# Kernel tuning notes

Measured on AMD Instinct MI355X. Metric: run time of the kernel, lower is better.

## Reference

```python
import jax, jax.numpy as jnp
import numpy as np

B, L, F, E, D, N_OUT, FC = 2048, 100, 64, 256, 256, 3, 128


def _lstm_cell(x, h, c, Wi, Wh, b):
    gates = x @ Wi + h @ Wh + b  # (B, 4H)
    i, f, g, o = jnp.split(gates, 4, axis=-1)
    c_new = jax.nn.sigmoid(f) * c + jax.nn.sigmoid(i) * jnp.tanh(g)
    h_new = jax.nn.sigmoid(o) * jnp.tanh(c_new)
    return h_new, c_new


def setup_inputs() -> dict:
    key = jax.random.key(0)
    ks = jax.random.split(key, 12)
    s = 0.05
    return {
        "x": jax.random.normal(ks[0], (B, L, F), jnp.float32),
        # encoder input-attention (shared across timesteps, as in [layer]*look_back)
        "Wa": jax.random.normal(ks[1], (F + E, F), jnp.float32) * s,
        "ba": jnp.zeros((F,), jnp.float32),
        # encoder LSTM cell
        "Wi": jax.random.normal(ks[2], (F, 4 * E), jnp.float32) * s,
        "Wh": jax.random.normal(ks[3], (E, 4 * E), jnp.float32) * s,
        "be": jnp.zeros((4 * E,), jnp.float32),
        # decoder temporal attention
        "Wd": jax.random.normal(ks[4], (E + D, D), jnp.float32) * s,
        "bd": jnp.zeros((D,), jnp.float32),
        "Wl": jax.random.normal(ks[5], (D, 1), jnp.float32) * s,
        "bl": jnp.zeros((1,), jnp.float32),
        # decoder LSTM cell
        "Wdi": jax.random.normal(ks[6], (E, 4 * D), jnp.float32) * s,
        "Wdh": jax.random.normal(ks[7], (D, 4 * D), jnp.float32) * s,
        "bdec": jnp.zeros((4 * D,), jnp.float32),
        # output head: tanh(D->FC) then tanh(FC->1)
        "Wf": jax.random.normal(ks[8], (D, FC), jnp.float32) * s,
        "bf": jnp.zeros((FC,), jnp.float32),
        "Wo": jax.random.normal(ks[9], (FC, 1), jnp.float32) * s,
        "bo": jnp.zeros((1,), jnp.float32),
    }


def reference(x, Wa, ba, Wi, Wh, be, Wd, bd, Wl, bl, Wdi, Wdh, bdec, Wf, bf, Wo, bo):
    # ---------- encoder: per-timestep input attention + LSTM cell ----------
    x_t = jnp.transpose(x, (1, 0, 2))  # (L, B, F)

    def enc_step(carry, xt):
        h, c = carry
        energies = jnp.tanh(jnp.concatenate([xt, h], axis=1) @ Wa + ba)  # (B, F)
        a = jax.nn.softmax(energies, axis=1)
        enc_in = a * xt  # attended input (B, F)
        h, c = _lstm_cell(enc_in, h, c, Wi, Wh, be)
        return (h, c), h

    h0 = jnp.zeros((B, E), x.dtype)
    c0 = jnp.zeros((B, E), x.dtype)
    _, enc_out = jax.lax.scan(enc_step, (h0, c0), x_t)  # (L, B, E)

    # ---------- decoder: temporal attention over encoder states + LSTM ----------
    h_d = jnp.zeros((B, D), x.dtype)
    c_d = jnp.zeros((B, D), x.dtype)
    outs = []
    for _ in range(N_OUT):  # small fixed output horizon
        con = jnp.broadcast_to(h_d[None, :, :], (L, B, D))
        en = jnp.tanh(jnp.concatenate([enc_out, con], axis=2) @ Wd + bd)  # (L, B, D)
        scores = en @ Wl + bl  # (L, B, 1)
        alpha = jax.nn.softmax(scores, axis=0)  # over time
        ctx = jnp.sum(alpha * enc_out, axis=0)  # (B, E)
        h_d, c_d = _lstm_cell(ctx, h_d, c_d, Wdi, Wdh, bdec)
        fc = jnp.tanh(h_d @ Wf + bf)  # (B, FC)
        outs.append(jnp.tanh(fc @ Wo + bo))  # (B, 1)
    return jnp.concatenate(outs, axis=1)  # (B, n_output)
```

## Files before the change

kernel.cpp:

```cpp
#include <hip/hip_runtime.h>
#include <math.h>

#define BB 2048
#define LL 100
#define FF 64
#define EE 256
#define DD 256
#define NOUT 3

#define COMP(v, i) ((i) == 0 ? (v).x : (i) == 1 ? (v).y : (i) == 2 ? (v).z : (v).w)

typedef unsigned short u16;
typedef unsigned int u32;
typedef __attribute__((ext_vector_type(8))) __bf16 bf16x8;
typedef __attribute__((ext_vector_type(4))) float f32x4;
typedef __attribute__((ext_vector_type(2))) float f32x2;

#define MFMA_(A, B, C) __builtin_amdgcn_mfma_f32_16x16x32_bf16((A), (B), (C), 0, 0, 0)

__device__ __forceinline__ float sigmoidf_(float x) {
    return 1.0f / (1.0f + expf(-x));
}
__device__ __forceinline__ float tanhf_(float x) {
    return 1.0f - 2.0f / (1.0f + expf(2.0f * x));
}
__device__ __forceinline__ u16 f2b_(float f) {
    u32 u = __float_as_uint(f);
    u = (u + 0x7FFFu + ((u >> 16) & 1u)) >> 16;
    return (u16)u;
}
__device__ __forceinline__ float b2f_(u16 b) {
    return __uint_as_float(((u32)b) << 16);
}
__device__ __forceinline__ u32 pack2_(float a, float b) {
    return (u32)f2b_(a) | ((u32)f2b_(b) << 16);
}
__device__ __forceinline__ f32x4 splat4(float b) {
    f32x4 v; v[0] = b; v[1] = b; v[2] = b; v[3] = b; return v;
}
__device__ __forceinline__ void split8(const float* v, uint4& H, uint4& L) {
    u16 h[8], lo[8];
    #pragma unroll
    for (int e = 0; e < 8; ++e) {
        h[e]  = f2b_(v[e]);
        lo[e] = f2b_(v[e] - b2f_(h[e]));
    }
    H = make_uint4((u32)h[0]  | ((u32)h[1]  << 16), (u32)h[2]  | ((u32)h[3]  << 16),
                   (u32)h[4]  | ((u32)h[5]  << 16), (u32)h[6]  | ((u32)h[7]  << 16));
    L = make_uint4((u32)lo[0] | ((u32)lo[1] << 16), (u32)lo[2] | ((u32)lo[3] << 16),
                   (u32)lo[4] | ((u32)lo[5] << 16), (u32)lo[6] | ((u32)lo[7] << 16));
}

#define AF(mt, kt, p, ln) (((((mt) * 10 + (kt)) * 2 + (p)) * 64 + (ln)) * 8)
#define AFX(mt, kt, p, ln) AF(mt, kt, p, (ln) ^ (((ln) >> 4) & 3))
#define AF2(mt, kt, p, ln) (((((mt) * 8 + (kt)) * 2 + (p)) * 64 + (ln)) * 8)

__global__ __launch_bounds__(64) void w_prep_all(
    const float* __restrict__ Wi, const float* __restrict__ Wh,
    const float* __restrict__ Wa, const float* __restrict__ Wd,
    u16* __restrict__ wp)
{
    const int bid = blockIdx.x;
    const int l   = threadIdx.x;

    float v[8];
    if (bid < 640) {
        const int nt = bid / 10, kt = bid - nt * 10;
        const int col = nt * 16 + (l & 15);
        #pragma unroll
        for (int e = 0; e < 8; ++e) {
            const int k = kt * 32 + ((l >> 4) << 3) + e;
            v[e] = (k < 64) ? Wi[(size_t)k * 1024 + col]
                            : Wh[(size_t)(k - 64) * 1024 + col];
        }
    } else if (bid < 680) {
        const int b2 = bid - 640;
        const int nt = b2 / 10, kt = b2 - nt * 10;
        const int col = nt * 16 + (l & 15);
        #pragma unroll
        for (int e = 0; e < 8; ++e) {
            const int k = kt * 32 + ((l >> 4) << 3) + e;
            v[e] = Wa[(size_t)k * 64 + col];
        }
    } else {
        const int b2 = bid - 680;
        const int nt = b2 >> 3, kt = b2 & 7;
        const int col = nt * 16 + (l & 15);
        #pragma unroll
        for (int e = 0; e < 8; ++e) {
            const int k = kt * 32 + ((l >> 4) << 3) + e;
            v[e] = Wd[(size_t)k * 256 + col];
        }
    }
    uint4 H, L;
    split8(v, H, L);
    *(uint4*)&wp[(size_t)bid * 1024 + (size_t)l * 8]       = H;
    *(uint4*)&wp[(size_t)bid * 1024 + 512 + (size_t)l * 8] = L;
}

__global__ __launch_bounds__(1024) void enc_mfma4(
    const float* __restrict__ x,
    const float* __restrict__ ba, const float* __restrict__ be,
    const u16* __restrict__ wp,
    float* __restrict__ enc_out,
    float* __restrict__ hbuf,
    u32* __restrict__ flags)
{
    __shared__ u16   aFrag[20480];
    __shared__ float x_s[32 * 68];
    __shared__ float e_s[32 * 68];
    __shared__ float gate_s[4][32][66];

    const int bid = blockIdx.x;
    const int g   = (bid & 7) | ((bid >> 5) << 3);
    const int p   = (bid >> 3) & 3;
    const int row0 = g * 32;
    const int tid = threadIdx.x;
    const int l   = tid & 63;
    const int w   = tid >> 6;

    for (int v = tid; v < 20480 / 2; v += 1024) ((u32*)aFrag)[v] = 0u;

    const int ntW = (w >> 2) * 16 + p * 4 + (w & 3);
    uint4 BhR[10];
    #pragma unroll
    for (int kt = 0; kt < 10; ++kt)
        BhR[kt] = *(const uint4*)&wp[(size_t)(ntW * 10 + kt) * 1024 + (size_t)l * 8];

    const float be_r = be[(size_t)ntW * 16 + (l & 15)];
    const float ba_r = (w < 8) ? ba[(w & 3) * 16 + (l & 15)] : 0.f;

    float c_state[2] = {0.f, 0.f};

    __syncthreads();

    for (int t = 0; t < LL; ++t) {
        if (t > 0) {
            if (tid == 0) {
                const u32 target = 4u * (u32)t;
                int guard = 0;
                while (__hip_atomic_load(&flags[g * 32], __ATOMIC_RELAXED,
                                         __HIP_MEMORY_SCOPE_AGENT) < target) {
                    __builtin_amdgcn_s_sleep(1);
                    if (++guard > 2000000) break;
                }
            }
            __syncthreads();
        }

        if (tid < 256) {
            const int kt2 = tid >> 7;
            const int mt  = (tid >> 6) & 1;
            const int l2  = tid & 63;
            const int row2 = mt * 16 + (l2 & 15);
            const int f0   = kt2 * 32 + ((l2 >> 4) << 3);
            const float* xp = x + (size_t)(row0 + row2) * (LL * FF) + (size_t)t * FF + f0;
            float4 xa = *(const float4*)xp;
            float4 xb = *(const float4*)(xp + 4);
            float v[8] = {xa.x, xa.y, xa.z, xa.w, xb.x, xb.y, xb.z, xb.w};
            uint4 H, L;
            split8(v, H, L);
            *(uint4*)&aFrag[AFX(mt, kt2, 0, l2)] = H;
            *(uint4*)&aFrag[AFX(mt, kt2, 1, l2)] = L;
            *(float4*)&x_s[row2 * 68 + f0]     = xa;
            *(float4*)&x_s[row2 * 68 + f0 + 4] = xb;
        } else if (t > 0) {
            const int v   = tid - 256;
            const int prl = v >> 8;
            const int vv  = v & 255;
            const int row = vv >> 3;
            const int i8  = vv & 7;
            const int ugp = (p + 1 + prl) & 3;
            const int u8  = ugp * 64 + i8 * 8;
            const float* hp_g = hbuf + ((size_t)((t - 1) & 1) * BB + row0 + row) * 256 + u8;
            f32x4 a4, b4;
            asm volatile("global_load_dwordx4 %0, %2, off sc0 sc1\n\t"
                         "global_load_dwordx4 %1, %3, off sc0 sc1\n\t"
                         "s_waitcnt vmcnt(0)"
                         : "=v"(a4), "=v"(b4)
                         : "v"(hp_g), "v"(hp_g + 4) : "memory");
            float v8[8] = {a4[0], a4[1], a4[2], a4[3], b4[0], b4[1], b4[2], b4[3]};
            uint4 H, L;
            split8(v8, H, L);
            const int mt = row >> 4, rowT = row & 15;
            const int kt_h = 2 + (u8 >> 5);
            const int g2   = (u8 & 31) >> 3;
            const int ln   = rowT + (g2 << 4);
            *(uint4*)&aFrag[AFX(mt, kt_h, 0, ln)] = H;
            *(uint4*)&aFrag[AFX(mt, kt_h, 1, ln)] = L;
        }
        __syncthreads();

        f32x4 acc0, acc1;

        if (w < 8) {
            const int mt  = w >> 2;
            const int nta = w & 3;
            f32x4 ea = splat4(ba_r);
            #pragma unroll
            for (int kt = 0; kt < 10; ++kt) {
                bf16x8 Ah = *(const bf16x8*)&aFrag[AFX(mt, kt, 0, l)];
                bf16x8 Al = *(const bf16x8*)&aFrag[AFX(mt, kt, 1, l)];
                const size_t o = (size_t)(640 + nta * 10 + kt) * 1024 + (size_t)l * 8;
                bf16x8 Bh = *(const bf16x8*)&wp[o];
                bf16x8 Bl = *(const bf16x8*)&wp[o + 512];
                ea = MFMA_(Ah, Bh, ea);
                ea = MFMA_(Al, Bh, ea);
                ea = MFMA_(Ah, Bl, ea);
            }
            const int colA = nta * 16 + (l & 15);
            #pragma unroll
            for (int r = 0; r < 4; ++r) {
                const int rowT = ((l >> 4) << 2) + r;
                e_s[(mt * 16 + rowT) * 68 + colA] = tanhf_(ea[r]);
            }
        } else {
            acc0 = splat4(be_r); acc1 = splat4(be_r);
            #pragma unroll
            for (int kt = 2; kt < 10; ++kt) {
                bf16x8 Ah0 = *(const bf16x8*)&aFrag[AFX(0, kt, 0, l)];
                bf16x8 Al0 = *(const bf16x8*)&aFrag[AFX(0, kt, 1, l)];
                bf16x8 Ah1 = *(const bf16x8*)&aFrag[AFX(1, kt, 0, l)];
                bf16x8 Al1 = *(const bf16x8*)&aFrag[AFX(1, kt, 1, l)];
                bf16x8 Bl  = *(const bf16x8*)&wp[(size_t)(ntW * 10 + kt) * 1024 + 512 + (size_t)l * 8];
                bf16x8 Bh  = __builtin_bit_cast(bf16x8, BhR[kt]);
                acc0 = MFMA_(Ah0, Bh, acc0);
                acc1 = MFMA_(Ah1, Bh, acc1);
                acc0 = MFMA_(Al0, Bh, acc0);
                acc1 = MFMA_(Al1, Bh, acc1);
                acc0 = MFMA_(Ah0, Bl, acc0);
                acc1 = MFMA_(Ah1, Bl, acc1);
            }
        }
        __syncthreads();

        if (w >= 8) {
            const int v2   = tid - 512;
            const int row2 = v2 >> 4;
            const int c4   = (v2 & 15) * 4;
            float4 ev = *(const float4*)&e_s[row2 * 68 + c4];
            float m = fmaxf(fmaxf(ev.x, ev.y), fmaxf(ev.z, ev.w));
            #pragma unroll
            for (int msk = 8; msk >= 1; msk >>= 1) m = fmaxf(m, __shfl_xor(m, msk, 64));
            float4 ex;
            ex.x = expf(ev.x - m); ex.y = expf(ev.y - m);
            ex.z = expf(ev.z - m); ex.w = expf(ev.w - m);
            float s = ex.x + ex.y + ex.z + ex.w;
            #pragma unroll
            for (int msk = 8; msk >= 1; msk >>= 1) s += __shfl_xor(s, msk, 64);
            const float inv = 1.f / s;
            float4 xv = *(const float4*)&x_s[row2 * 68 + c4];
            float ein[4] = { ex.x * inv * xv.x, ex.y * inv * xv.y,
                             ex.z * inv * xv.z, ex.w * inv * xv.w };
            const int mt   = row2 >> 4;
            const int rowT = row2 & 15;
            const int kt   = c4 >> 5;
            const int g2   = (c4 & 31) >> 3;
            const int e0   = c4 & 7;
            const int ln   = rowT + (g2 << 4);
            ushort4 h4, l4;
            #pragma unroll
            for (int e = 0; e < 4; ++e) {
                u16 hh = f2b_(ein[e]);
                u16 ll = f2b_(ein[e] - b2f_(hh));
                if (e == 0) { h4.x = hh; l4.x = ll; } else if (e == 1) { h4.y = hh; l4.y = ll; }
                else if (e == 2) { h4.z = hh; l4.z = ll; } else { h4.w = hh; l4.w = ll; }
            }
            *(ushort4*)&aFrag[AFX(mt, kt, 0, ln) + e0] = h4;
            *(ushort4*)&aFrag[AFX(mt, kt, 1, ln) + e0] = l4;
        } else {
            acc0 = splat4(be_r); acc1 = splat4(be_r);
            #pragma unroll
            for (int kt = 2; kt < 10; ++kt) {
                bf16x8 Ah0 = *(const bf16x8*)&aFrag[AFX(0, kt, 0, l)];
                bf16x8 Al0 = *(const bf16x8*)&aFrag[AFX(0, kt, 1, l)];
                bf16x8 Ah1 = *(const bf16x8*)&aFrag[AFX(1, kt, 0, l)];
                bf16x8 Al1 = *(const bf16x8*)&aFrag[AFX(1, kt, 1, l)];
                bf16x8 Bl  = *(const bf16x8*)&wp[(size_t)(ntW * 10 + kt) * 1024 + 512 + (size_t)l * 8];
                bf16x8 Bh  = __builtin_bit_cast(bf16x8, BhR[kt]);
                acc0 = MFMA_(Ah0, Bh, acc0);
                acc1 = MFMA_(Ah1, Bh, acc1);
                acc0 = MFMA_(Al0, Bh, acc0);
                acc1 = MFMA_(Al1, Bh, acc1);
                acc0 = MFMA_(Ah0, Bl, acc0);
                acc1 = MFMA_(Ah1, Bl, acc1);
            }
        }
        __syncthreads();

        #pragma unroll
        for (int kt = 0; kt < 2; ++kt) {
            bf16x8 Ah0 = *(const bf16x8*)&aFrag[AFX(0, kt, 0, l)];
            bf16x8 Al0 = *(const bf16x8*)&aFrag[AFX(0, kt, 1, l)];
            bf16x8 Ah1 = *(const bf16x8*)&aFrag[AFX(1, kt, 0, l)];
            bf16x8 Al1 = *(const bf16x8*)&aFrag[AFX(1, kt, 1, l)];
            bf16x8 Bl  = *(const bf16x8*)&wp[(size_t)(ntW * 10 + kt) * 1024 + 512 + (size_t)l * 8];
            bf16x8 Bh  = __builtin_bit_cast(bf16x8, BhR[kt]);
            acc0 = MFMA_(Ah0, Bh, acc0);
            acc1 = MFMA_(Ah1, Bh, acc1);
            acc0 = MFMA_(Al0, Bh, acc0);
            acc1 = MFMA_(Al1, Bh, acc1);
            acc0 = MFMA_(Ah0, Bl, acc0);
            acc1 = MFMA_(Ah1, Bl, acc1);
        }
        {
            const int gate = w >> 2;
            const int ulb  = (w & 3) * 16 + (l & 15);
            #pragma unroll
            for (int r = 0; r < 4; ++r) {
                const int rT = ((l >> 4) << 2) + r;
                gate_s[gate][rT][ulb]      = acc0[r];
                gate_s[gate][16 + rT][ulb] = acc1[r];
            }
        }
        __syncthreads();

        {
            const int row = tid >> 5;
            const int q2  = (tid & 31) * 2;
            float gi0 = gate_s[0][row][q2], gi1 = gate_s[0][row][q2 + 1];
            float gf0 = gate_s[1][row][q2], gf1 = gate_s[1][row][q2 + 1];
            float gg0 = gate_s[2][row][q2], gg1 = gate_s[2][row][q2 + 1];
            float go0 = gate_s[3][row][q2], go1 = gate_s[3][row][q2 + 1];
            float cv0 = sigmoidf_(gf0) * c_state[0] + sigmoidf_(gi0) * tanhf_(gg0);
            float cv1 = sigmoidf_(gf1) * c_state[1] + sigmoidf_(gi1) * tanhf_(gg1);
            c_state[0] = cv0; c_state[1] = cv1;
            float hv0 = sigmoidf_(go0) * tanhf_(cv0);
            float hv1 = sigmoidf_(go1) * tanhf_(cv1);
            const int u_g = p * 64 + q2;
            *(float2*)&enc_out[((size_t)t * BB + row0 + row) * 256 + u_g]
                = make_float2(hv0, hv1);
            float* hp_g = hbuf + ((size_t)(t & 1) * BB + row0 + row) * 256 + u_g;
            f32x2 hv2; hv2[0] = hv0; hv2[1] = hv1;
            asm volatile("global_store_dwordx2 %0, %1, off sc0 sc1"
                         :: "v"(hp_g), "v"(hv2) : "memory");
            const int mt = row >> 4, rowT = row & 15;
            const int kt_h = 2 + (u_g >> 5);
            const int g2   = (u_g & 31) >> 3;
            const int ln   = rowT + (g2 << 4);
            const int e    = u_g & 7;
            ((u32*)aFrag)[(AFX(mt, kt_h, 0, ln) + e) >> 1] = pack2_(hv0, hv1);
            u16 h0 = f2b_(hv0), h1 = f2b_(hv1);
            ((u32*)aFrag)[(AFX(mt, kt_h, 1, ln) + e) >> 1] =
                (u32)f2b_(hv0 - b2f_(h0)) | ((u32)f2b_(hv1 - b2f_(h1)) << 16);
        }
        asm volatile("s_waitcnt vmcnt(0)" ::: "memory");
        __syncthreads();
        if (tid == 0)
            __hip_atomic_fetch_add(&flags[g * 32], 1u, __ATOMIC_RELEASE,
                                   __HIP_MEMORY_SCOPE_AGENT);
    }
}

__global__ __launch_bounds__(256) void gemm_ep_mfma(
    const float* __restrict__ A, const u16* __restrict__ wp,
    float* __restrict__ C)
{
    __shared__ u16   aF[2 * 8 * 2 * 64 * 8];
    __shared__ float c_s[32 * 260];
    const int m0  = blockIdx.x * 32;
    const int tid = threadIdx.x;
    const int l   = tid & 63;
    const int w   = tid >> 6;

    for (int s = tid; s < 1024; s += 256) {
        const int mt = s >> 9, kt = (s >> 6) & 7, l2 = s & 63;
        const int row2 = mt * 16 + (l2 & 15);
        const int k0   = kt * 32 + ((l2 >> 4) << 3);
        const float* ap = A + (size_t)(m0 + row2) * 256 + k0;
        float4 xa = *(const float4*)ap;
        float4 xb = *(const float4*)(ap + 4);
        float v[8] = {xa.x, xa.y, xa.z, xa.w, xb.x, xb.y, xb.z, xb.w};
        uint4 H, L;
        split8(v, H, L);
        *(uint4*)&aF[AF2(mt, kt, 0, l2)] = H;
        *(uint4*)&aF[AF2(mt, kt, 1, l2)] = L;
    }
    __syncthreads();

    f32x4 acc[2][4];
    #pragma unroll
    for (int mt = 0; mt < 2; ++mt)
        #pragma unroll
        for (int j = 0; j < 4; ++j) acc[mt][j] = splat4(0.f);

    #pragma unroll
    for (int kt = 0; kt < 8; ++kt) {
        bf16x8 Ah0 = *(const bf16x8*)&aF[AF2(0, kt, 0, l)];
        bf16x8 Al0 = *(const bf16x8*)&aF[AF2(0, kt, 1, l)];
        bf16x8 Ah1 = *(const bf16x8*)&aF[AF2(1, kt, 0, l)];
        bf16x8 Al1 = *(const bf16x8*)&aF[AF2(1, kt, 1, l)];
        #pragma unroll
        for (int j = 0; j < 4; ++j) {
            const int nt = w * 4 + j;
            const u16* bt = wp + (size_t)(680 + nt * 8 + kt) * 1024 + (size_t)l * 8;
            bf16x8 Bh = *(const bf16x8*)bt;
            bf16x8 Bl = *(const bf16x8*)(bt + 512);
            acc[0][j] = MFMA_(Ah0, Bh, acc[0][j]);
            acc[1][j] = MFMA_(Ah1, Bh, acc[1][j]);
            acc[0][j] = MFMA_(Al0, Bh, acc[0][j]);
            acc[1][j] = MFMA_(Al1, Bh, acc[1][j]);
            acc[0][j] = MFMA_(Ah0, Bl, acc[0][j]);
            acc[1][j] = MFMA_(Ah1, Bl, acc[1][j]);
        }
    }

    #pragma unroll
    for (int mt = 0; mt < 2; ++mt)
        #pragma unroll
        for (int j = 0; j < 4; ++j) {
            const int col = (w * 4 + j) * 16 + (l & 15);
            #pragma unroll
            for (int r = 0; r < 4; ++r) {
                const int row = mt * 16 + ((l >> 4) << 2) + r;
                c_s[row * 260 + col] = acc[mt][j][r];
            }
        }
    __syncthreads();
    for (int v = tid; v < 32 * 64; v += 256) {
        const int row = v >> 6, c4 = (v & 63) << 2;
        *(float4*)&C[(size_t)(m0 + row) * 256 + c4] = *(const float4*)&c_s[row * 260 + c4];
    }
}

__global__ __launch_bounds__(256) void gemm_nk256(
    const float* __restrict__ A, const float* __restrict__ W,
    const float* __restrict__ bias, float* __restrict__ C, int skip_gemm)
{
    __shared__ float a_s[32 * 256];
    const int m0   = blockIdx.x * 32;
    const int tid  = threadIdx.x;
    const int lane = tid & 63;
    const int rg   = tid >> 6;
    const int n0   = lane * 4;

    float4 bias4 = make_float4(0.f, 0.f, 0.f, 0.f);
    if (bias) bias4 = *(const float4*)&bias[n0];

    if (skip_gemm) {
        #pragma unroll
        for (int r = 0; r < 8; ++r)
            *(float4*)&C[(size_t)(m0 + rg * 8 + r) * 256 + n0] = bias4;
        return;
    }

    for (int v = tid; v < 32 * 64; v += 256)
        ((float4*)a_s)[v] = ((const float4*)(A + (size_t)m0 * 256))[v];
    __syncthreads();

    float4 acc[8];
    #pragma unroll
    for (int r = 0; r < 8; ++r) acc[r] = bias4;

    #pragma unroll 2
    for (int k = 0; k < 256; k += 4) {
        float4 wv[4];
        #pragma unroll
        for (int kk = 0; kk < 4; ++kk)
            wv[kk] = *(const float4*)&W[(size_t)(k + kk) * 256 + n0];
        float4 av[8];
        #pragma unroll
        for (int r = 0; r < 8; ++r)
            av[r] = *(const float4*)&a_s[(rg * 8 + r) * 256 + k];
        #pragma unroll
        for (int kk = 0; kk < 4; ++kk) {
            #pragma unroll
            for (int r = 0; r < 8; ++r) {
                float e = COMP(av[r], kk);
                acc[r].x += e * wv[kk].x; acc[r].y += e * wv[kk].y;
                acc[r].z += e * wv[kk].z; acc[r].w += e * wv[kk].w;
            }
        }
    }
    #pragma unroll
    for (int r = 0; r < 8; ++r)
        *(float4*)&C[(size_t)(m0 + rg * 8 + r) * 256 + n0] = acc[r];
}

__global__ __launch_bounds__(256) void pack_ep(
    float* A, const float* __restrict__ W, u16* epOut, int packed)
{
    __shared__ float a_s[32 * 256];
    const int m0   = blockIdx.x * 32;
    const int tid  = threadIdx.x;
    const int lane = tid & 63;
    const int rg   = tid >> 6;
    const int n0   = lane * 4;

    for (int v = tid; v < 32 * 64; v += 256)
        ((float4*)a_s)[v] = ((const float4*)(A + (size_t)m0 * 256))[v];
    __syncthreads();

    float4 acc[8];
    #pragma unroll
    for (int r = 0; r < 8; ++r) acc[r] = make_float4(0.f, 0.f, 0.f, 0.f);

    #pragma unroll 2
    for (int k = 0; k < 256; k += 4) {
        float4 wv[4];
        #pragma unroll
        for (int kk = 0; kk < 4; ++kk)
            wv[kk] = *(const float4*)&W[(size_t)(k + kk) * 256 + n0];
        float4 av[8];
        #pragma unroll
        for (int r = 0; r < 8; ++r)
            av[r] = *(const float4*)&a_s[(rg * 8 + r) * 256 + k];
        #pragma unroll
        for (int kk = 0; kk < 4; ++kk) {
            #pragma unroll
            for (int r = 0; r < 8; ++r) {
                float e = COMP(av[r], kk);
                acc[r].x += e * wv[kk].x; acc[r].y += e * wv[kk].y;
                acc[r].z += e * wv[kk].z; acc[r].w += e * wv[kk].w;
            }
        }
    }

    u16* epu = packed ? (u16*)A : epOut;
    #pragma unroll
    for (int r = 0; r < 8; ++r) {
        const size_t row = (size_t)(m0 + rg * 8 + r);
        ushort4 o;
        o.x = f2b_(acc[r].x); o.y = f2b_(acc[r].y);
        o.z = f2b_(acc[r].z); o.w = f2b_(acc[r].w);
        u16* dst = packed ? (epu + row * 512 + 256 + n0)
                          : (epu + row * 256 + n0);
        *(ushort4*)dst = o;
    }

    if (packed) {
        u32* ab = (u32*)A;
        for (int v = tid; v < 32 * 128; v += 256) {
            const int row = v >> 7, j = v & 127;
            float2 f = *(const float2*)&a_s[(row << 8) + (j << 1)];
            ab[((size_t)(m0 + row)) * 256 + j] = pack2_(f.x, f.y);
        }
    }
}

__global__ __launch_bounds__(512) void scores_sm_ctx(
    const float* __restrict__ ep, const float* __restrict__ hp,
    const float* __restrict__ Wl, const float* __restrict__ enc_out,
    float* __restrict__ ctx)
{
    __shared__ float hp_s[8 * 256];
    __shared__ float al_s[8 * 100];
    const int b0  = blockIdx.x * 8;
    const int tid = threadIdx.x;

    for (int v = tid; v < 512; v += 512)
        ((float4*)hp_s)[v] = ((const float4*)(hp + (size_t)b0 * 256))[v];
    __syncthreads();

    {
        const int r = tid >> 6;
        const int g = tid & 63;
        const float4 wl4 = *(const float4*)&Wl[g * 4];
        const float4 h4  = *(const float4*)&hp_s[r * 256 + g * 4];
        for (int l = 0; l < LL; ++l) {
            const float* er = ep + ((size_t)l * BB + b0 + r) * 256;
            float4 e4 = *(const float4*)&er[g * 4];
            float p = tanhf_(e4.x + h4.x) * wl4.x + tanhf_(e4.y + h4.y) * wl4.y
                    + tanhf_(e4.z + h4.z) * wl4.z + tanhf_(e4.w + h4.w) * wl4.w;
            #pragma unroll
            for (int msk = 32; msk >= 1; msk >>= 1) p += __shfl_xor(p, msk, 64);
            if (g == 0) al_s[r * 100 + l] = p;
        }
    }
    __syncthreads();
    if (tid < 8) {
        float m = -1e30f;
        for (int l = 0; l < LL; ++l) m = fmaxf(m, al_s[tid * 100 + l]);
        float s = 0.f;
        for (int l = 0; l < LL; ++l) { float e = expf(al_s[tid * 100 + l] - m); al_s[tid * 100 + l] = e; s += e; }
        float inv = 1.f / s;
        for (int l = 0; l < LL; ++l) al_s[tid * 100 + l] *= inv;
    }
    __syncthreads();
    {
        const int u  = tid & 255;
        const int rh = tid >> 8;
        float acc[4] = {};
        for (int l = 0; l < LL; ++l) {
            const float* er2 = enc_out + (size_t)l * (BB * 256)
                             + (size_t)(b0 + rh * 4) * 256 + u;
            #pragma unroll
            for (int j = 0; j < 4; ++j)
                acc[j] += al_s[(rh * 4 + j) * 100 + l] * er2[j * 256];
        }
        #pragma unroll
        for (int j = 0; j < 4; ++j)
            ctx[(size_t)(b0 + rh * 4 + j) * 256 + u] = acc[j];
    }
}

__global__ __launch_bounds__(256) void scores_ep_b16(
    const u16* __restrict__ ep, const float* __restrict__ hp,
    const float* __restrict__ Wl, float* __restrict__ scores,
    int sstr, int soff)
{
    __shared__ float hp_s[8 * 256];
    const int b0  = blockIdx.x * 8;
    const int l0  = blockIdx.y * 20;
    const int tid = threadIdx.x;
    const int r   = tid >> 5;
    const int g   = tid & 31;

    for (int v = tid; v < 512; v += 256)
        ((float4*)hp_s)[v] = ((const float4*)(hp + (size_t)b0 * 256))[v];
    __syncthreads();

    const float4 wl0 = *(const float4*)&Wl[g * 4];
    const float4 wl1 = *(const float4*)&Wl[128 + g * 4];
    const float4 h0  = *(const float4*)&hp_s[r * 256 + g * 4];
    const float4 h1  = *(const float4*)&hp_s[r * 256 + 128 + g * 4];

    #pragma unroll 2
    for (int li = 0; li < 20; ++li) {
        const u16* er = ep + ((size_t)(l0 + li) * BB + b0 + r) * sstr + soff;
        ushort4 u0 = *(const ushort4*)&er[g * 4];
        ushort4 u1 = *(const ushort4*)&er[128 + g * 4];
        float p = tanhf_(b2f_(u0.x) + h0.x) * wl0.x + tanhf_(b2f_(u0.y) + h0.y) * wl0.y
                + tanhf_(b2f_(u0.z) + h0.z) * wl0.z + tanhf_(b2f_(u0.w) + h0.w) * wl0.w
                + tanhf_(b2f_(u1.x) + h1.x) * wl1.x + tanhf_(b2f_(u1.y) + h1.y) * wl1.y
                + tanhf_(b2f_(u1.z) + h1.z) * wl1.z + tanhf_(b2f_(u1.w) + h1.w) * wl1.w;
        #pragma unroll
        for (int msk = 16; msk >= 1; msk >>= 1) p += __shfl_xor(p, msk, 64);
        if (g == 0) scores[(size_t)(l0 + li) * BB + b0 + r] = p;
    }
}

__global__ __launch_bounds__(256) void softmax_ctx(
    const float* __restrict__ scores, const float* __restrict__ enc_out,
    float* __restrict__ ctx)
{
    __shared__ float al_s[8 * 100];
    const int b0  = blockIdx.x * 8;
    const int tid = threadIdx.x;
    for (int v = tid; v < 800; v += 256) {
        int r = v / 100, l = v - r * 100;
        al_s[r * 100 + l] = scores[(size_t)l * BB + b0 + r];
    }
    __syncthreads();
    if (tid < 8) {
        float m = -1e30f;
        for (int l = 0; l < LL; ++l) m = fmaxf(m, al_s[tid * 100 + l]);
        float s = 0.f;
        for (int l = 0; l < LL; ++l) { float e = expf(al_s[tid * 100 + l] - m); al_s[tid * 100 + l] = e; s += e; }
        float inv = 1.f / s;
        for (int l = 0; l < LL; ++l) al_s[tid * 100 + l] *= inv;
    }
    __syncthreads();
    float acc[8] = {};
    for (int l = 0; l < LL; ++l) {
        const float* er = enc_out + (size_t)l * (BB * 256) + (size_t)b0 * 256 + tid;
        #pragma unroll
        for (int r = 0; r < 8; ++r) acc[r] += al_s[r * 100 + l] * er[r * 256];
    }
    for (int r = 0; r < 8; ++r) ctx[(size_t)(b0 + r) * 256 + tid] = acc[r];
}

__global__ __launch_bounds__(256) void softmax_ctx_b16(
    const float* __restrict__ scores, const u16* __restrict__ encp,
    float* __restrict__ ctx)
{
    __shared__ float al_s[8 * 100];
    const int b0  = blockIdx.x * 8;
    const int tid = threadIdx.x;
    for (int v = tid; v < 800; v += 256) {
        int r = v / 100, l = v - r * 100;
        al_s[r * 100 + l] = scores[(size_t)l * BB + b0 + r];
    }
    __syncthreads();
    if (tid < 8) {
        float m = -1e30f;
        for (int l = 0; l < LL; ++l) m = fmaxf(m, al_s[tid * 100 + l]);
        float s = 0.f;
        for (int l = 0; l < LL; ++l) { float e = expf(al_s[tid * 100 + l] - m); al_s[tid * 100 + l] = e; s += e; }
        float inv = 1.f / s;
        for (int l = 0; l < LL; ++l) al_s[tid * 100 + l] *= inv;
    }
    __syncthreads();
    float acc[8] = {};
    for (int l = 0; l < LL; ++l) {
        const u16* er = encp + ((size_t)l * BB + b0) * 512 + tid;
        #pragma unroll
        for (int r = 0; r < 8; ++r) acc[r] += al_s[r * 100 + l] * b2f_(er[r * 512]);
    }
    for (int r = 0; r < 8; ++r) ctx[(size_t)(b0 + r) * 256 + tid] = acc[r];
}

__global__ __launch_bounds__(512) void dec_step(
    const float* __restrict__ ctxp,
    const float* __restrict__ Wdi, const float* __restrict__ Wdh,
    const float* __restrict__ bdec,
    float* __restrict__ hd, float* __restrict__ c_st, int first)
{
    __shared__ float ct_s[8 * 256];
    __shared__ float hd_s[8 * 256];
    __shared__ float gate_s[2][8 * 1024];
    const int row0 = blockIdx.x * 8;
    const int tid  = threadIdx.x;
    const int lane = tid & 63, w = tid >> 6;
    const int half = tid >> 8;
    const int ct   = tid & 255;
    const int c0   = ct * 4;

    ((float4*)ct_s)[tid] = ((const float4*)(ctxp + (size_t)row0 * 256))[tid];
    if (!first)
        ((float4*)hd_s)[tid] = ((const float4*)(hd + (size_t)row0 * 256))[tid];
    __syncthreads();

    float4 acc[8];
    {
        float4 b4 = *(const float4*)&bdec[c0];
        float4 bias4 = (half == 0) ? b4 : make_float4(0.f, 0.f, 0.f, 0.f);
        #pragma unroll
        for (int r = 0; r < 8; ++r) acc[r] = bias4;
    }
    if (half == 0) {
        const float* wP = Wdi + c0;
        #pragma unroll 2
        for (int ch = 0; ch < 64; ++ch) {
            const int k0 = ch * 4;
            float4 w0 = *(const float4*)&wP[(size_t)(k0 + 0) * 1024];
            float4 w1 = *(const float4*)&wP[(size_t)(k0 + 1) * 1024];
            float4 w2 = *(const float4*)&wP[(size_t)(k0 + 2) * 1024];
            float4 w3 = *(const float4*)&wP[(size_t)(k0 + 3) * 1024];
            #pragma unroll
            for (int r = 0; r < 8; ++r) {
                float4 av = *(const float4*)&ct_s[r * 256 + k0];
                acc[r].x += av.x * w0.x; acc[r].y += av.x * w0.y;
                acc[r].z += av.x * w0.z; acc[r].w += av.x * w0.w;
                acc[r].x += av.y * w1.x; acc[r].y += av.y * w1.y;
                acc[r].z += av.y * w1.z; acc[r].w += av.y * w1.w;
                acc[r].x += av.z * w2.x; acc[r].y += av.z * w2.y;
                acc[r].z += av.z * w2.z; acc[r].w += av.z * w2.w;
                acc[r].x += av.w * w3.x; acc[r].y += av.w * w3.y;
                acc[r].z += av.w * w3.z; acc[r].w += av.w * w3.w;
            }
        }
    } else if (!first) {
        const float* wP = Wdh + c0;
        #pragma unroll 2
        for (int ch = 0; ch < 64; ++ch) {
            const int k0 = ch * 4;
            float4 w0 = *(const float4*)&wP[(size_t)(k0 + 0) * 1024];
            float4 w1 = *(const float4*)&wP[(size_t)(k0 + 1) * 1024];
            float4 w2 = *(const float4*)&wP[(size_t)(k0 + 2) * 1024];
            float4 w3 = *(const float4*)&wP[(size_t)(k0 + 3) * 1024];
            #pragma unroll
            for (int r = 0; r < 8; ++r) {
                float4 av = *(const float4*)&hd_s[r * 256 + k0];
                acc[r].x += av.x * w0.x; acc[r].y += av.x * w0.y;
                acc[r].z += av.x * w0.z; acc[r].w += av.x * w0.w;
                acc[r].x += av.y * w1.x; acc[r].y += av.y * w1.y;
                acc[r].z += av.y * w1.z; acc[r].w += av.y * w1.w;
                acc[r].x += av.z * w2.x; acc[r].y += av.z * w2.y;
                acc[r].z += av.z * w2.z; acc[r].w += av.z * w2.w;
                acc[r].x += av.w * w3.x; acc[r].y += av.w * w3.y;
                acc[r].z += av.w * w3.z; acc[r].w += av.w * w3.w;
            }
        }
    }
    #pragma unroll
    for (int r = 0; r < 8; ++r)
        *(float4*)&gate_s[half][r * 1024 + c0] = acc[r];
    __syncthreads();

    {
        const float* g0 = &gate_s[0][w * 1024 + lane * 4];
        const float* g1 = &gate_s[1][w * 1024 + lane * 4];
        float4 giA = *(const float4*)&g0[0],   giB = *(const float4*)&g1[0];
        float4 gfA = *(const float4*)&g0[256], gfB = *(const float4*)&g1[256];
        float4 ggA = *(const float4*)&g0[512], ggB = *(const float4*)&g1[512];
        float4 goA = *(const float4*)&g0[768], goB = *(const float4*)&g1[768];
        size_t ci = (size_t)(row0 + w) * 256 + lane * 4;
        float4 c4 = first ? make_float4(0.f, 0.f, 0.f, 0.f)
                          : *(const float4*)&c_st[ci];
        float cc[4] = { c4.x, c4.y, c4.z, c4.w };
        float gi[4] = { giA.x + giB.x, giA.y + giB.y, giA.z + giB.z, giA.w + giB.w };
        float gf[4] = { gfA.x + gfB.x, gfA.y + gfB.y, gfA.z + gfB.z, gfA.w + gfB.w };
        float gg[4] = { ggA.x + ggB.x, ggA.y + ggB.y, ggA.z + ggB.z, ggA.w + ggB.w };
        float go[4] = { goA.x + goB.x, goA.y + goB.y, goA.z + goB.z, goA.w + goB.w };
        float4 cn, hn;
        #pragma unroll
        for (int uu = 0; uu < 4; ++uu) {
            float cv = sigmoidf_(gf[uu]) * cc[uu] + sigmoidf_(gi[uu]) * tanhf_(gg[uu]);
            float hv = sigmoidf_(go[uu]) * tanhf_(cv);
            if (uu == 0) { cn.x = cv; hn.x = hv; } else if (uu == 1) { cn.y = cv; hn.y = hv; }
            else if (uu == 2) { cn.z = cv; hn.z = hv; } else { cn.w = cv; hn.w = hv; }
        }
        *(float4*)&c_st[ci] = cn;
        *(float4*)&hd[ci]   = hn;
    }
}

__global__ __launch_bounds__(256) void head_k(
    const float* __restrict__ hd, const float* __restrict__ Wf,
    const float* __restrict__ bf, const float* __restrict__ Wo,
    const float* __restrict__ bo, float* __restrict__ out, int step)
{
    __shared__ float hd_s[16 * 256];
    __shared__ float fc_s[16 * 128];
    const int b0  = blockIdx.x * 16;
    const int tid = threadIdx.x;
    {
        const float4* hg = (const float4*)(hd + (size_t)b0 * 256);
        for (int i = tid; i < 1024; i += 256) ((float4*)hd_s)[i] = hg[i];
    }
    __syncthreads();
    {
        const int f = tid & 127, rg = tid >> 7;
        float acc[8];
        float bfv = bf[f];
        #pragma unroll
        for (int rr = 0; rr < 8; ++rr) acc[rr] = bfv;
        const float* wp = Wf + f;
        #pragma unroll 2
        for (int k = 0; k < 256; ++k) {
            float wv = wp[k * 128];
            #pragma unroll
            for (int rr = 0; rr < 8; ++rr) acc[rr] += hd_s[(rg * 8 + rr) * 256 + k] * wv;
        }
        for (int rr = 0; rr < 8; ++rr) fc_s[(rg * 8 + rr) * 128 + f] = tanhf_(acc[rr]);
    }
    __syncthreads();
    {
        const int lane = tid & 63, w = tid >> 6;
        const float bov = bo[0];
        #pragma unroll
        for (int rr = 0; rr < 4; ++rr) {
            int r = w * 4 + rr;
            float p = fc_s[r * 128 + lane] * Wo[lane] + fc_s[r * 128 + 64 + lane] * Wo[64 + lane];
            #pragma unroll
            for (int msk = 32; msk >= 1; msk >>= 1) p += __shfl_xor(p, msk, 64);
            if (lane == 0) out[(size_t)(b0 + r) * NOUT + step] = tanhf_(p + bov);
        }
    }
}

extern "C" void kernel_launch(void* const* d_in, const int* in_sizes, int n_in,
                              void* d_out, int out_size, void* d_ws, size_t ws_size,
                              hipStream_t stream)
{
    const float* x    = (const float*)d_in[0];
    const float* Wa   = (const float*)d_in[1];
    const float* ba   = (const float*)d_in[2];
    const float* Wi   = (const float*)d_in[3];
    const float* Wh   = (const float*)d_in[4];
    const float* be   = (const float*)d_in[5];
    const float* Wd   = (const float*)d_in[6];
    const float* bd   = (const float*)d_in[7];
    const float* Wl   = (const float*)d_in[8];
    const float* bl   = (const float*)d_in[9];
    const float* Wdi  = (const float*)d_in[10];
    const float* Wdh  = (const float*)d_in[11];
    const float* bdec = (const float*)d_in[12];
    const float* Wf   = (const float*)d_in[13];
    const float* bf   = (const float*)d_in[14];
    const float* Wo   = (const float*)d_in[15];
    const float* bo   = (const float*)d_in[16];
    float* out = (float*)d_out;

    const size_t f_enc    = (size_t)LL * BB * EE;
    const size_t f_state  = (size_t)BB * EE;
    const size_t f_scores = (size_t)LL * BB;
    const size_t need3 = (f_enc + 3 * f_state + f_scores) * sizeof(float);
    const size_t need2 = need3 + f_enc * sizeof(u16);
    const size_t need1 = need3 + f_enc * sizeof(float);

    float* ws      = (float*)d_ws;
    float* enc_out = ws;
    float* hd      = enc_out + f_enc;
    float* c_d     = hd + f_state;
    float* ctx     = c_d + f_state;
    float* scores  = ctx + f_state;
    float* ep32    = scores + f_scores;
    u16*   ep16    = (u16*)(scores + f_scores);
    float* hp      = ctx;
    u16*   wprep   = (u16*)ctx;
    float* hbuf    = hd;
    u32*   flags   = (u32*)scores;

    if (ws_size < need3) return;
    const int tier = (ws_size >= need1) ? 1 : (ws_size >= need2) ? 2 : 3;

    hipMemsetAsync(flags, 0, 64 * 32 * sizeof(u32), stream);
    w_prep_all<<<808, 64, 0, stream>>>(Wi, Wh, Wa, Wd, wprep);
    enc_mfma4<<<256, 1024, 0, stream>>>(x, ba, be, wprep, enc_out, hbuf, flags);

    if (tier == 1)
        gemm_ep_mfma<<<(LL * BB) / 32, 256, 0, stream>>>(enc_out, wprep, ep32);
    else
        pack_ep<<<(LL * BB) / 32, 256, 0, stream>>>(
            enc_out, Wd, ep16, tier == 3 ? 1 : 0);

    for (int s = 0; s < NOUT; ++s) {
        gemm_nk256<<<BB / 32, 256, 0, stream>>>(
            hd, Wd + 256 * 256, bd, hp, s == 0);
        if (tier == 1) {
            scores_sm_ctx<<<BB / 8, 512, 0, stream>>>(ep32, hp, Wl, enc_out, ctx);
        } else if (tier == 2) {
            scores_ep_b16<<<dim3(BB / 8, 5), 256, 0, stream>>>(ep16, hp, Wl, scores, 256, 0);
            softmax_ctx<<<BB / 8, 256, 0, stream>>>(scores, enc_out, ctx);
        } else {
            scores_ep_b16<<<dim3(BB / 8, 5), 256, 0, stream>>>(
                (const u16*)enc_out, hp, Wl, scores, 512, 256);
            softmax_ctx_b16<<<BB / 8, 256, 0, stream>>>(scores, (const u16*)enc_out, ctx);
        }
        dec_step<<<BB / 8, 512, 0, stream>>>(ctx, Wdi, Wdh, bdec, hd, c_d, s == 0);
        head_k<<<BB / 16, 256, 0, stream>>>(hd, Wf, bf, Wo, bo, out, s);
    }
}
```

Baseline: 2.249 ms.

## Keep Wh low-half weights in registers and store encoder/projection outputs as bf16

The encoder kernel now preloads the low bf16 halves of the recurrent weights into registers alongside the high halves, so the inner MFMA loops no longer reload them from global memory each timestep. It also adds a launch-bounds occupancy hint. The tier-1 projection GEMM now writes its output and a copy of the encoder states in bf16, and the decoder attention kernel reads those bf16 buffers, halving the memory traffic of the three decoder steps. Register pressure in the encoder rises, which could cause spills, and the bf16 storage lowers accuracy.

```diff
diff --git a/kernel.cpp b/kernel.cpp
--- a/kernel.cpp
+++ b/kernel.cpp
@@ -98,7 +98,7 @@
     *(uint4*)&wp[(size_t)bid * 1024 + 512 + (size_t)l * 8] = L;
 }
 
-__global__ __launch_bounds__(1024) void enc_mfma4(
+__global__ __launch_bounds__(1024, 4) void enc_mfma4(
     const float* __restrict__ x,
     const float* __restrict__ ba, const float* __restrict__ be,
     const u16* __restrict__ wp,
@@ -122,10 +122,13 @@
     for (int v = tid; v < 20480 / 2; v += 1024) ((u32*)aFrag)[v] = 0u;
 
     const int ntW = (w >> 2) * 16 + p * 4 + (w & 3);
-    uint4 BhR[10];
+    uint4 BhR[10], BlR[10];
     #pragma unroll
-    for (int kt = 0; kt < 10; ++kt)
-        BhR[kt] = *(const uint4*)&wp[(size_t)(ntW * 10 + kt) * 1024 + (size_t)l * 8];
+    for (int kt = 0; kt < 10; ++kt) {
+        const size_t o = (size_t)(ntW * 10 + kt) * 1024 + (size_t)l * 8;
+        BhR[kt] = *(const uint4*)&wp[o];
+        BlR[kt] = *(const uint4*)&wp[o + 512];
+    }
 
     const float be_r = be[(size_t)ntW * 16 + (l & 15)];
     const float ba_r = (w < 8) ? ba[(w & 3) * 16 + (l & 15)] : 0.f;
@@ -222,8 +225,8 @@
                 bf16x8 Al0 = *(const bf16x8*)&aFrag[AFX(0, kt, 1, l)];
                 bf16x8 Ah1 = *(const bf16x8*)&aFrag[AFX(1, kt, 0, l)];
                 bf16x8 Al1 = *(const bf16x8*)&aFrag[AFX(1, kt, 1, l)];
-                bf16x8 Bl  = *(const bf16x8*)&wp[(size_t)(ntW * 10 + kt) * 1024 + 512 + (size_t)l * 8];
                 bf16x8 Bh  = __builtin_bit_cast(bf16x8, BhR[kt]);
+                bf16x8 Bl  = __builtin_bit_cast(bf16x8, BlR[kt]);
                 acc0 = MFMA_(Ah0, Bh, acc0);
                 acc1 = MFMA_(Ah1, Bh, acc1);
                 acc0 = MFMA_(Al0, Bh, acc0);
@@ -276,8 +279,8 @@
                 bf16x8 Al0 = *(const bf16x8*)&aFrag[AFX(0, kt, 1, l)];
                 bf16x8 Ah1 = *(const bf16x8*)&aFrag[AFX(1, kt, 0, l)];
                 bf16x8 Al1 = *(const bf16x8*)&aFrag[AFX(1, kt, 1, l)];
-                bf16x8 Bl  = *(const bf16x8*)&wp[(size_t)(ntW * 10 + kt) * 1024 + 512 + (size_t)l * 8];
                 bf16x8 Bh  = __builtin_bit_cast(bf16x8, BhR[kt]);
+                bf16x8 Bl  = __builtin_bit_cast(bf16x8, BlR[kt]);
                 acc0 = MFMA_(Ah0, Bh, acc0);
                 acc1 = MFMA_(Ah1, Bh, acc1);
                 acc0 = MFMA_(Al0, Bh, acc0);
@@ -294,8 +297,8 @@
             bf16x8 Al0 = *(const bf16x8*)&aFrag[AFX(0, kt, 1, l)];
             bf16x8 Ah1 = *(const bf16x8*)&aFrag[AFX(1, kt, 0, l)];
             bf16x8 Al1 = *(const bf16x8*)&aFrag[AFX(1, kt, 1, l)];
-            bf16x8 Bl  = *(const bf16x8*)&wp[(size_t)(ntW * 10 + kt) * 1024 + 512 + (size_t)l * 8];
             bf16x8 Bh  = __builtin_bit_cast(bf16x8, BhR[kt]);
+            bf16x8 Bl  = __builtin_bit_cast(bf16x8, BlR[kt]);
             acc0 = MFMA_(Ah0, Bh, acc0);
             acc1 = MFMA_(Ah1, Bh, acc1);
             acc0 = MFMA_(Al0, Bh, acc0);
@@ -352,9 +355,9 @@
     }
 }
 
-__global__ __launch_bounds__(256) void gemm_ep_mfma(
+__global__ __launch_bounds__(256) void gemm_ep_mfma_b16(
     const float* __restrict__ A, const u16* __restrict__ wp,
-    float* __restrict__ C)
+    u16* __restrict__ epb, u16* __restrict__ encb)
 {
     __shared__ u16   aF[2 * 8 * 2 * 64 * 8];
     __shared__ float c_s[32 * 260];
@@ -375,6 +378,8 @@
         split8(v, H, L);
         *(uint4*)&aF[AF2(mt, kt, 0, l2)] = H;
         *(uint4*)&aF[AF2(mt, kt, 1, l2)] = L;
+        u32* eb = (u32*)encb + ((size_t)(m0 + row2) << 7) + (k0 >> 1);
+        eb[0] = H.x; eb[1] = H.y; eb[2] = H.z; eb[3] = H.w;
     }
     __syncthreads();
 
@@ -417,9 +422,10 @@
             }
         }
     __syncthreads();
-    for (int v = tid; v < 32 * 64; v += 256) {
-        const int row = v >> 6, c4 = (v & 63) << 2;
-        *(float4*)&C[(size_t)(m0 + row) * 256 + c4] = *(const float4*)&c_s[row * 260 + c4];
+    for (int v = tid; v < 32 * 128; v += 256) {
+        const int row = v >> 7, j = v & 127;
+        float2 f = *(const float2*)&c_s[row * 260 + (j << 1)];
+        ((u32*)epb)[((size_t)(m0 + row) << 7) + j] = pack2_(f.x, f.y);
     }
 }
 
@@ -538,9 +544,9 @@
     }
 }
 
-__global__ __launch_bounds__(512) void scores_sm_ctx(
-    const float* __restrict__ ep, const float* __restrict__ hp,
-    const float* __restrict__ Wl, const float* __restrict__ enc_out,
+__global__ __launch_bounds__(512) void scores_sm_ctx_b16(
+    const u16* __restrict__ epb, const float* __restrict__ hp,
+    const float* __restrict__ Wl, const u16* __restrict__ encb,
     float* __restrict__ ctx)
 {
     __shared__ float hp_s[8 * 256];
@@ -558,10 +564,12 @@
         const float4 wl4 = *(const float4*)&Wl[g * 4];
         const float4 h4  = *(const float4*)&hp_s[r * 256 + g * 4];
         for (int l = 0; l < LL; ++l) {
-            const float* er = ep + ((size_t)l * BB + b0 + r) * 256;
-            float4 e4 = *(const float4*)&er[g * 4];
-            float p = tanhf_(e4.x + h4.x) * wl4.x + tanhf_(e4.y + h4.y) * wl4.y
-                    + tanhf_(e4.z + h4.z) * wl4.z + tanhf_(e4.w + h4.w) * wl4.w;
+            const u16* er = epb + ((size_t)l * BB + b0 + r) * 256;
+            ushort4 e4 = *(const ushort4*)&er[g * 4];
+            float p = tanhf_(b2f_(e4.x) + h4.x) * wl4.x
+                    + tanhf_(b2f_(e4.y) + h4.y) * wl4.y
+                    + tanhf_(b2f_(e4.z) + h4.z) * wl4.z
+                    + tanhf_(b2f_(e4.w) + h4.w) * wl4.w;
             #pragma unroll
             for (int msk = 32; msk >= 1; msk >>= 1) p += __shfl_xor(p, msk, 64);
             if (g == 0) al_s[r * 100 + l] = p;
@@ -582,11 +590,11 @@
         const int rh = tid >> 8;
         float acc[4] = {};
         for (int l = 0; l < LL; ++l) {
-            const float* er2 = enc_out + (size_t)l * (BB * 256)
-                             + (size_t)(b0 + rh * 4) * 256 + u;
+            const u16* er2 = encb + (size_t)l * (BB * 256)
+                           + (size_t)(b0 + rh * 4) * 256 + u;
             #pragma unroll
             for (int j = 0; j < 4; ++j)
-                acc[j] += al_s[(rh * 4 + j) * 100 + l] * er2[j * 256];
+                acc[j] += al_s[(rh * 4 + j) * 100 + l] * b2f_(er2[j * 256]);
         }
         #pragma unroll
         for (int j = 0; j < 4; ++j)
@@ -876,7 +884,8 @@
     float* c_d     = hd + f_state;
     float* ctx     = c_d + f_state;
     float* scores  = ctx + f_state;
-    float* ep32    = scores + f_scores;
+    u16*   epb     = (u16*)(scores + f_scores);
+    u16*   encb    = epb + f_enc;
     u16*   ep16    = (u16*)(scores + f_scores);
     float* hp      = ctx;
     u16*   wprep   = (u16*)ctx;
@@ -891,7 +900,8 @@
     enc_mfma4<<<256, 1024, 0, stream>>>(x, ba, be, wprep, enc_out, hbuf, flags);
 
     if (tier == 1)
-        gemm_ep_mfma<<<(LL * BB) / 32, 256, 0, stream>>>(enc_out, wprep, ep32);
+        gemm_ep_mfma_b16<<<(LL * BB) / 32, 256, 0, stream>>>(
+            enc_out, wprep, epb, encb);
     else
         pack_ep<<<(LL * BB) / 32, 256, 0, stream>>>(
             enc_out, Wd, ep16, tier == 3 ? 1 : 0);
@@ -900,7 +910,7 @@
         gemm_nk256<<<BB / 32, 256, 0, stream>>>(
             hd, Wd + 256 * 256, bd, hp, s == 0);
         if (tier == 1) {
-            scores_sm_ctx<<<BB / 8, 512, 0, stream>>>(ep32, hp, Wl, enc_out, ctx);
+            scores_sm_ctx_b16<<<BB / 8, 512, 0, stream>>>(epb, hp, Wl, encb, ctx);
         } else if (tier == 2) {
             scores_ep_b16<<<dim3(BB / 8, 5), 256, 0, stream>>>(ep16, hp, Wl, scores, 256, 0);
             softmax_ctx<<<BB / 8, 256, 0, stream>>>(scores, enc_out, ctx);
```

Measured after the change: 2.697 ms. 19.9% more time.
